# Optimization experiments

Measured on AMD Instinct MI355X. Metric: run time of the kernel, lower is better.

The kernel has to match this reference:

```python
import jax, jax.numpy as jnp
import numpy as np

P_DROP = 0.2  # matches nn.Dropout(0.2) in the module __init__ (forward's dropout_p arg is unused)
DROPOUT_KEY = jax.random.key(42)  # deterministic dropout mask for reproducible baseline


def setup_inputs() -> dict:
    key = jax.random.key(0)
    kq, kk, kv = jax.random.split(key, 3)
    B, Sq, Sk, D, Dv = 4, 4096, 4096, 64, 64
    return {
        "q": jax.random.normal(kq, (B, Sq, D), dtype=jnp.float32),
        "k": jax.random.normal(kk, (B, Sk, D), dtype=jnp.float32),
        "v": jax.random.normal(kv, (B, Sk, Dv), dtype=jnp.float32),
        "scale_factor": 1,
        "dropout_p": 0,
    }


def reference(q, k, v, scale_factor, dropout_p):
    # qk = q @ k^T, scaled  -> [B, Sq, Sk] (full attention matrix, as in the original)
    qk = jnp.einsum("bqd,bkd->bqk", q, k) * scale_factor
    probs = jax.nn.softmax(qk, axis=-1)
    # dropout (train-mode nn.Dropout(p=0.2)): deterministic mask, inverted scaling
    keep = jax.random.bernoulli(DROPOUT_KEY, 1.0 - P_DROP, probs.shape)
    probs = jnp.where(keep, probs / (1.0 - P_DROP), 0.0)
    # output = probs @ v -> [B, Sq, Dv]
    return jnp.einsum("bqk,bkd->bqd", probs, v)
```

## Files before the change

kernel.cpp:

```cpp
#include <hip/hip_runtime.h>
#include <hip/hip_bf16.h>
#include <stdint.h>

typedef __attribute__((ext_vector_type(8))) _Float16 f16x8;
typedef __attribute__((ext_vector_type(4))) float f32x4;

static constexpr int BATCH = 4;
static constexpr int SEQ = 4096;
static constexpr int DIM = 64;
static constexpr uint32_t KEEP_THRESH = 0xCCCCCE00u;
static constexpr int NSPLIT = 4;
static constexpr int TILES_TOTAL = SEQ / 64;
static constexpr int TILES_PER_SPLIT = TILES_TOTAL / NSPLIT;

static constexpr size_t ONUM_BYTES = (size_t)BATCH * 64 * NSPLIT * 64 * 64 * 4;
static constexpr size_t ML_BYTES   = (size_t)BATCH * 64 * NSPLIT * 64 * 2 * 4;
static constexpr size_t WS_NEEDED  = ONUM_BYTES + ML_BYTES;

__device__ __forceinline__ uint32_t rotl32(uint32_t x, int r) {
  return __builtin_rotateleft32(x, (uint32_t)r);
}

__device__ __forceinline__ bool tf_keep(uint32_t j) {
  const uint32_t k1 = 42u;
  const uint32_t k2 = 0x1BD11BDAu ^ k1;
  uint32_t x1 = j + k1;
  uint32_t x0 = x1;
  x1 = rotl32(x1, 13) ^ x0;
  x0 += x1; x1 = rotl32(x1, 15) ^ x0;
  x0 += x1; x1 = rotl32(x1, 26) ^ x0;
  x0 += x1; x1 = rotl32(x1, 6)  ^ x0;
  x0 += k1;      x1 += k2 + 1u;
  x0 += x1; x1 = rotl32(x1, 17) ^ x0;
  x0 += x1; x1 = rotl32(x1, 29) ^ x0;
  x0 += x1; x1 = rotl32(x1, 16) ^ x0;
  x0 += x1; x1 = rotl32(x1, 24) ^ x0;
  x0 += k2;      x1 += 2u;
  x0 += x1; x1 = rotl32(x1, 13) ^ x0;
  x0 += x1; x1 = rotl32(x1, 15) ^ x0;
  x0 += x1; x1 = rotl32(x1, 26) ^ x0;
  x0 += x1; x1 = rotl32(x1, 6)  ^ x0;
   x1 += k1 + 3u;
  x0 += x1; x1 = rotl32(x1, 17) ^ x0;
  x0 += x1; x1 = rotl32(x1, 29) ^ x0;
  x0 += x1; x1 = rotl32(x1, 16) ^ x0;
  x0 += x1; x1 = rotl32(x1, 24) ^ x0;
  x0 += k1;      x1 += k2 + 4u;
  x0 += x1; x1 = rotl32(x1, 13) ^ x0;
  x0 += x1; x1 = rotl32(x1, 15) ^ x0;
  x0 += x1; x1 = rotl32(x1, 26) ^ x0;
  x0 += x1; x1 = rotl32(x1, 6)  ^ x0;
  x0 += k2;      x1 += 5u;
  return (x0 ^ x1) < KEEP_THRESH;
}

template<bool PARTIAL>
__global__ __launch_bounds__(256, 4) void attn_kernel(
    const float* __restrict__ Q, const float* __restrict__ K, const float* __restrict__ V,
    const uint32_t* __restrict__ scale_raw,
    float* __restrict__ Out, float* __restrict__ onum, float* __restrict__ ml)
{
  __shared__ __align__(16) _Float16 Khi[64 * 72];
  __shared__ __align__(16) _Float16 Klo[64 * 72];
  __shared__ __align__(16) _Float16 Vld[64 * 72];
  __shared__ __align__(16) _Float16 Pld[4][16 * 72];

  const int b   = blockIdx.y;
  const int q0  = blockIdx.x * 64;
  const int tid = threadIdx.x;
  const int w    = tid >> 6;
  const int lane = tid & 63;
  const int l15  = lane & 15;
  const int l4   = lane >> 4;

  float scale;
  {
    uint32_t sb = *scale_raw;
    int e = (int)((sb >> 23) & 0xFFu);
    if (sb == 0u) scale = 0.0f;
    else if (e == 0 || e == 255) scale = (float)(int)sb;
    else scale = __uint_as_float(sb);
  }

  const int qw = q0 + w * 16;

  uint32_t rcb[4];
#pragma unroll
  for (int r = 0; r < 4; ++r)
    rcb[r] = ((uint32_t)(b * SEQ + qw + l4 * 4 + r)) * (uint32_t)SEQ;

  f16x8 aqh[2], aql[2];
#pragma unroll
  for (int c = 0; c < 2; ++c) {
    const float* qp = Q + ((size_t)(b * SEQ + qw + l15)) * DIM + l4 * 8 + 32 * c;
    f16x8 h, l;
#pragma unroll
    for (int j = 0; j < 8; ++j) {
      float f = qp[j];
      _Float16 fh = (_Float16)f;
      h[j] = fh;
      l[j] = (_Float16)(f - (float)fh);
    }
    aqh[c] = h; aql[c] = l;
  }

  float m_r[4], l_r[4];
  f32x4 Oacc[4];
#pragma unroll
  for (int r = 0; r < 4; ++r) { m_r[r] = -INFINITY; l_r[r] = 0.0f; }
#pragma unroll
  for (int n = 0; n < 4; ++n) Oacc[n] = f32x4{0.f, 0.f, 0.f, 0.f};

  const int t0 = PARTIAL ? (int)blockIdx.z * TILES_PER_SPLIT : 0;
  const int nt = PARTIAL ? TILES_PER_SPLIT : TILES_TOTAL;

  for (int kt = 0; kt < nt; ++kt) {
    const int kbase = (t0 + kt) * 64;
    __syncthreads();
#pragma unroll
    for (int i = 0; i < 4; ++i) {
      int flat = tid + i * 256;
      int row = flat >> 4;
      int col = (flat & 15) * 4;
      const float* kp = K + ((size_t)(b * SEQ + kbase + row)) * DIM + col;
      const float* vp = V + ((size_t)(b * SEQ + kbase + row)) * DIM + col;
      float4 kf = *(const float4*)kp;
      float4 vf = *(const float4*)vp;
      _Float16 h0 = (_Float16)kf.x, h1 = (_Float16)kf.y,
               h2 = (_Float16)kf.z, h3 = (_Float16)kf.w;
      *(ushort4*)&Khi[row * 72 + col] = ushort4{
        __builtin_bit_cast(unsigned short, h0), __builtin_bit_cast(unsigned short, h1),
        __builtin_bit_cast(unsigned short, h2), __builtin_bit_cast(unsigned short, h3)};
      _Float16 l0 = (_Float16)(kf.x - (float)h0), l1 = (_Float16)(kf.y - (float)h1),
               l2 = (_Float16)(kf.z - (float)h2), l3 = (_Float16)(kf.w - (float)h3);
      *(ushort4*)&Klo[row * 72 + col] = ushort4{
        __builtin_bit_cast(unsigned short, l0), __builtin_bit_cast(unsigned short, l1),
        __builtin_bit_cast(unsigned short, l2), __builtin_bit_cast(unsigned short, l3)};
      Vld[(col + 0) * 72 + row] = (_Float16)vf.x;
      Vld[(col + 1) * 72 + row] = (_Float16)vf.y;
      Vld[(col + 2) * 72 + row] = (_Float16)vf.z;
      Vld[(col + 3) * 72 + row] = (_Float16)vf.w;
    }
    __syncthreads();

    f32x4 s[4];
#pragma unroll
    for (int n = 0; n < 4; ++n) {
      f32x4 acc = f32x4{0.f, 0.f, 0.f, 0.f};
#pragma unroll
      for (int c = 0; c < 2; ++c) {
        int off = (16 * n + l15) * 72 + l4 * 8 + 32 * c;
        f16x8 bh = *(const f16x8*)&Khi[off];
        f16x8 bl = *(const f16x8*)&Klo[off];
        acc = __builtin_amdgcn_mfma_f32_16x16x32_f16(aqh[c], bh, acc, 0, 0, 0);
        acc = __builtin_amdgcn_mfma_f32_16x16x32_f16(aqh[c], bl, acc, 0, 0, 0);
        acc = __builtin_amdgcn_mfma_f32_16x16x32_f16(aql[c], bh, acc, 0, 0, 0);
      }
#pragma unroll
      for (int r = 0; r < 4; ++r) acc[r] *= scale;
      s[n] = acc;
    }

    uint32_t kbits = 0;
#pragma unroll
    for (int n = 0; n < 4; ++n) {
      uint32_t cb = (uint32_t)(kbase + l15 + 16 * n);
#pragma unroll
      for (int r = 0; r < 4; ++r) {
        if (tf_keep(rcb[r] + cb)) kbits |= (1u << (n * 4 + r));
      }
    }

    float mnew[4];
#pragma unroll
    for (int r = 0; r < 4; ++r) {
      mnew[r] = fmaxf(fmaxf(s[0][r], s[1][r]), fmaxf(s[2][r], s[3][r]));
#pragma unroll
      for (int off = 1; off < 16; off <<= 1)
        mnew[r] = fmaxf(mnew[r], __shfl_xor(mnew[r], off, 64));
    }

    float corr[4];
#pragma unroll
    for (int r = 0; r < 4; ++r) {
      float mn = fmaxf(m_r[r], mnew[r]);
      corr[r] = __expf(m_r[r] - mn);
      m_r[r] = mn;
      l_r[r] *= corr[r];
    }
#pragma unroll
    for (int n = 0; n < 4; ++n)
#pragma unroll
      for (int r = 0; r < 4; ++r) Oacc[n][r] *= corr[r];

    float psum[4] = {0.f, 0.f, 0.f, 0.f};
    _Float16* pw = &Pld[w][0];
#pragma unroll
    for (int n = 0; n < 4; ++n) {
#pragma unroll
      for (int r = 0; r < 4; ++r) {
        float e = __expf(s[n][r] - m_r[r]);
        psum[r] += e;
        float p = ((kbits >> (n * 4 + r)) & 1u) ? e : 0.0f;
        pw[(l4 * 4 + r) * 72 + l15 + 16 * n] = (_Float16)p;
      }
    }
#pragma unroll
    for (int r = 0; r < 4; ++r) {
#pragma unroll
      for (int off = 1; off < 16; off <<= 1)
        psum[r] += __shfl_xor(psum[r], off, 64);
      l_r[r] += psum[r];
    }

    asm volatile("s_waitcnt lgkmcnt(0)" ::: "memory");
    __builtin_amdgcn_sched_barrier(0);

    f16x8 pa[2];
#pragma unroll
    for (int c = 0; c < 2; ++c)
      pa[c] = *(const f16x8*)&pw[l15 * 72 + l4 * 8 + 32 * c];
#pragma unroll
    for (int n = 0; n < 4; ++n) {
#pragma unroll
      for (int c = 0; c < 2; ++c) {
        f16x8 bv = *(const f16x8*)&Vld[(l15 + 16 * n) * 72 + l4 * 8 + 32 * c];
        Oacc[n] = __builtin_amdgcn_mfma_f32_16x16x32_f16(pa[c], bv, Oacc[n], 0, 0, 0);
      }
    }
  }

  if (PARTIAL) {
    const int pb = ((b * 64 + (int)blockIdx.x) * NSPLIT + (int)blockIdx.z);
    float* op = onum + (size_t)pb * 4096;
#pragma unroll
    for (int r = 0; r < 4; ++r) {
      int row64 = w * 16 + l4 * 4 + r;
#pragma unroll
      for (int n = 0; n < 4; ++n)
        op[row64 * 64 + l15 + 16 * n] = Oacc[n][r];
      if (l15 == 0) {
        ml[(size_t)pb * 128 + row64 * 2 + 0] = m_r[r];
        ml[(size_t)pb * 128 + row64 * 2 + 1] = l_r[r];
      }
    }
  } else {
#pragma unroll
    for (int r = 0; r < 4; ++r) {
      float inv = 1.0f / (l_r[r] * 0.8f);
      int qg = qw + l4 * 4 + r;
      float* op = Out + ((size_t)(b * SEQ + qg)) * DIM + l15;
#pragma unroll
      for (int n = 0; n < 4; ++n)
        op[16 * n] = Oacc[n][r] * inv;
    }
  }
}

__global__ __launch_bounds__(256) void combine_kernel(
    const float* __restrict__ onum, const float* __restrict__ ml, float* __restrict__ Out)
{
  const int w = threadIdx.x >> 6;
  const int lane = threadIdx.x & 63;
  const int rid = blockIdx.x * 4 + w;
  const int b = rid >> 12;
  const int qrow = rid & 4095;
  const int qb = qrow >> 6;
  const int r64 = qrow & 63;
  const int pb0 = (b * 64 + qb) * NSPLIT;

  float m[NSPLIT], l[NSPLIT];
  float M = -INFINITY;
#pragma unroll
  for (int s = 0; s < NSPLIT; ++s) {
    m[s] = ml[(size_t)(pb0 + s) * 128 + r64 * 2 + 0];
    l[s] = ml[(size_t)(pb0 + s) * 128 + r64 * 2 + 1];
    M = fmaxf(M, m[s]);
  }
  float L = 0.0f, acc = 0.0f;
#pragma unroll
  for (int s = 0; s < NSPLIT; ++s) {
    float sc = __expf(m[s] - M);
    L += l[s] * sc;
    acc += onum[(size_t)(pb0 + s) * 4096 + r64 * 64 + lane] * sc;
  }
  Out[(size_t)rid * 64 + lane] = acc / (L * 0.8f);
}

extern "C" void kernel_launch(void* const* d_in, const int* in_sizes, int n_in,
                              void* d_out, int out_size, void* d_ws, size_t ws_size,
                              hipStream_t stream) {
  const float* Q = (const float*)d_in[0];
  const float* K = (const float*)d_in[1];
  const float* V = (const float*)d_in[2];
  const uint32_t* scale_raw = (const uint32_t*)d_in[3];
  float* Out = (float*)d_out;

  if (ws_size >= WS_NEEDED) {
    float* onum = (float*)d_ws;
    float* ml = (float*)((char*)d_ws + ONUM_BYTES);
    attn_kernel<true><<<dim3(64, BATCH, NSPLIT), 256, 0, stream>>>(
        Q, K, V, scale_raw, nullptr, onum, ml);
    combine_kernel<<<SEQ * BATCH / 4, 256, 0, stream>>>(onum, ml, Out);
  } else {
    attn_kernel<false><<<dim3(64, BATCH, 1), 256, 0, stream>>>(
        Q, K, V, scale_raw, Out, nullptr, nullptr);
  }
}
```

Measured before the change: 197.9 us.

## Swizzle LDS layouts, use ds_swizzle reductions, skip rescale, split KV eightfold

Replaces padded LDS arrays with XOR-swizzled 64-wide layouts for K hi/lo, a transposed V and P, to avoid bank conflicts and cut LDS footprint. V is now loaded column-wise so each thread writes a contiguous ushort4 into the transposed tile instead of four scalar stores. Row max and sum reductions use ds_swizzle instead of shfl_xor, the online-softmax rescale is skipped when no row max grows, and rotations use alignbit. The KV split goes from 4 to 8 when workspace allows, with launch bounds raised to 5 waves, which means more partial traffic in the combine step in exchange for more parallelism.

Result: slower. 228.1 us (+15.3%).

```diff
diff --git a/kernel.cpp b/kernel.cpp
--- a/kernel.cpp
+++ b/kernel.cpp
@@ -9,61 +9,75 @@
 static constexpr int SEQ = 4096;
 static constexpr int DIM = 64;
 static constexpr uint32_t KEEP_THRESH = 0xCCCCCE00u;
-static constexpr int NSPLIT = 4;
-static constexpr int TILES_TOTAL = SEQ / 64;
-static constexpr int TILES_PER_SPLIT = TILES_TOTAL / NSPLIT;
-
-static constexpr size_t ONUM_BYTES = (size_t)BATCH * 64 * NSPLIT * 64 * 64 * 4;
-static constexpr size_t ML_BYTES   = (size_t)BATCH * 64 * NSPLIT * 64 * 2 * 4;
-static constexpr size_t WS_NEEDED  = ONUM_BYTES + ML_BYTES;
-
-__device__ __forceinline__ uint32_t rotl32(uint32_t x, int r) {
-  return __builtin_rotateleft32(x, (uint32_t)r);
-}
+
+static constexpr size_t PB_BYTES = (64 * 64 + 128) * 4;
+static __host__ __device__ constexpr size_t ws_need(int ns) {
+  return (size_t)BATCH * 64 * ns * PB_BYTES;
+}
+static __host__ __device__ constexpr size_t onum_bytes(int ns) {
+  return (size_t)BATCH * 64 * ns * 64 * 64 * 4;
+}
+
+__device__ __forceinline__ int lds_swz(int row, int colbyte) {
+  return row * 128 + (colbyte ^ ((row & 7) << 4));
+}
+
+#define ROTL(x, r) (__builtin_amdgcn_alignbit((x), (x), 32 - (r)))
 
 __device__ __forceinline__ bool tf_keep(uint32_t j) {
   const uint32_t k1 = 42u;
   const uint32_t k2 = 0x1BD11BDAu ^ k1;
   uint32_t x1 = j + k1;
   uint32_t x0 = x1;
-  x1 = rotl32(x1, 13) ^ x0;
-  x0 += x1; x1 = rotl32(x1, 15) ^ x0;
-  x0 += x1; x1 = rotl32(x1, 26) ^ x0;
-  x0 += x1; x1 = rotl32(x1, 6)  ^ x0;
+  x1 = ROTL(x1, 13) ^ x0;
+  x0 += x1; x1 = ROTL(x1, 15) ^ x0;
+  x0 += x1; x1 = ROTL(x1, 26) ^ x0;
+  x0 += x1; x1 = ROTL(x1, 6)  ^ x0;
   x0 += k1;      x1 += k2 + 1u;
-  x0 += x1; x1 = rotl32(x1, 17) ^ x0;
-  x0 += x1; x1 = rotl32(x1, 29) ^ x0;
-  x0 += x1; x1 = rotl32(x1, 16) ^ x0;
-  x0 += x1; x1 = rotl32(x1, 24) ^ x0;
+  x0 += x1; x1 = ROTL(x1, 17) ^ x0;
+  x0 += x1; x1 = ROTL(x1, 29) ^ x0;
+  x0 += x1; x1 = ROTL(x1, 16) ^ x0;
+  x0 += x1; x1 = ROTL(x1, 24) ^ x0;
   x0 += k2;      x1 += 2u;
-  x0 += x1; x1 = rotl32(x1, 13) ^ x0;
-  x0 += x1; x1 = rotl32(x1, 15) ^ x0;
-  x0 += x1; x1 = rotl32(x1, 26) ^ x0;
-  x0 += x1; x1 = rotl32(x1, 6)  ^ x0;
-   x1 += k1 + 3u;
-  x0 += x1; x1 = rotl32(x1, 17) ^ x0;
-  x0 += x1; x1 = rotl32(x1, 29) ^ x0;
-  x0 += x1; x1 = rotl32(x1, 16) ^ x0;
-  x0 += x1; x1 = rotl32(x1, 24) ^ x0;
+  x0 += x1; x1 = ROTL(x1, 13) ^ x0;
+  x0 += x1; x1 = ROTL(x1, 15) ^ x0;
+  x0 += x1; x1 = ROTL(x1, 26) ^ x0;
+  x0 += x1; x1 = ROTL(x1, 6)  ^ x0;
+    x1 += k1 + 3u;
+  x0 += x1; x1 = ROTL(x1, 17) ^ x0;
+  x0 += x1; x1 = ROTL(x1, 29) ^ x0;
+  x0 += x1; x1 = ROTL(x1, 16) ^ x0;
+  x0 += x1; x1 = ROTL(x1, 24) ^ x0;
   x0 += k1;      x1 += k2 + 4u;
-  x0 += x1; x1 = rotl32(x1, 13) ^ x0;
-  x0 += x1; x1 = rotl32(x1, 15) ^ x0;
-  x0 += x1; x1 = rotl32(x1, 26) ^ x0;
-  x0 += x1; x1 = rotl32(x1, 6)  ^ x0;
+  x0 += x1; x1 = ROTL(x1, 13) ^ x0;
+  x0 += x1; x1 = ROTL(x1, 15) ^ x0;
+  x0 += x1; x1 = ROTL(x1, 26) ^ x0;
+  x0 += x1; x1 = ROTL(x1, 6)  ^ x0;
   x0 += k2;      x1 += 5u;
   return (x0 ^ x1) < KEEP_THRESH;
 }
 
-template<bool PARTIAL>
-__global__ __launch_bounds__(256, 4) void attn_kernel(
+template<int IMM>
+__device__ __forceinline__ float swz_max(float x) {
+  int y = __builtin_amdgcn_ds_swizzle(__float_as_int(x), IMM);
+  return fmaxf(x, __int_as_float(y));
+}
+template<int IMM>
+__device__ __forceinline__ float swz_add(float x) {
+  int y = __builtin_amdgcn_ds_swizzle(__float_as_int(x), IMM);
+  return x + __int_as_float(y);
+}
+
+template<bool PARTIAL, int NS>
+__global__ __launch_bounds__(256, 5) void attn_kernel(
     const float* __restrict__ Q, const float* __restrict__ K, const float* __restrict__ V,
     const uint32_t* __restrict__ scale_raw,
     float* __restrict__ Out, float* __restrict__ onum, float* __restrict__ ml)
 {
-  __shared__ __align__(16) _Float16 Khi[64 * 72];
-  __shared__ __align__(16) _Float16 Klo[64 * 72];
-  __shared__ __align__(16) _Float16 Vld[64 * 72];
-  __shared__ __align__(16) _Float16 Pld[4][16 * 72];
+  __shared__ __align__(16) _Float16 Khi[64 * 64];
+  __shared__ __align__(16) _Float16 Klo[64 * 64];
+  __shared__ __align__(16) _Float16 Vt[64 * 64];
+  __shared__ __align__(16) _Float16 Pld[4][16 * 64];
 
   const int b   = blockIdx.y;
   const int q0  = blockIdx.x * 64;
@@ -111,35 +125,40 @@
 #pragma unroll
   for (int n = 0; n < 4; ++n) Oacc[n] = f32x4{0.f, 0.f, 0.f, 0.f};
 
-  const int t0 = PARTIAL ? (int)blockIdx.z * TILES_PER_SPLIT : 0;
-  const int nt = PARTIAL ? TILES_PER_SPLIT : TILES_TOTAL;
+  const int nt = PARTIAL ? (SEQ / 64) / NS : SEQ / 64;
+  const int t0 = PARTIAL ? (int)blockIdx.z * nt : 0;
+
+  const int vd = tid & 63;
+  const int vq = tid >> 6;
 
   for (int kt = 0; kt < nt; ++kt) {
     const int kbase = (t0 + kt) * 64;
     __syncthreads();
 #pragma unroll
     for (int i = 0; i < 4; ++i) {
-      int flat = tid + i * 256;
-      int row = flat >> 4;
-      int col = (flat & 15) * 4;
-      const float* kp = K + ((size_t)(b * SEQ + kbase + row)) * DIM + col;
-      const float* vp = V + ((size_t)(b * SEQ + kbase + row)) * DIM + col;
-      float4 kf = *(const float4*)kp;
-      float4 vf = *(const float4*)vp;
+      int k  = (tid >> 4) + 16 * i;
+      int d0 = (tid & 15) * 4;
+      float4 kf = *(const float4*)(K + ((size_t)(b * SEQ + kbase + k)) * DIM + d0);
       _Float16 h0 = (_Float16)kf.x, h1 = (_Float16)kf.y,
                h2 = (_Float16)kf.z, h3 = (_Float16)kf.w;
-      *(ushort4*)&Khi[row * 72 + col] = ushort4{
+      *(ushort4*)((char*)Khi + lds_swz(k, d0 * 2)) = ushort4{
         __builtin_bit_cast(unsigned short, h0), __builtin_bit_cast(unsigned short, h1),
         __builtin_bit_cast(unsigned short, h2), __builtin_bit_cast(unsigned short, h3)};
       _Float16 l0 = (_Float16)(kf.x - (float)h0), l1 = (_Float16)(kf.y - (float)h1),
                l2 = (_Float16)(kf.z - (float)h2), l3 = (_Float16)(kf.w - (float)h3);
-      *(ushort4*)&Klo[row * 72 + col] = ushort4{
+      *(ushort4*)((char*)Klo + lds_swz(k, d0 * 2)) = ushort4{
         __builtin_bit_cast(unsigned short, l0), __builtin_bit_cast(unsigned short, l1),
         __builtin_bit_cast(unsigned short, l2), __builtin_bit_cast(unsigned short, l3)};
-      Vld[(col + 0) * 72 + row] = (_Float16)vf.x;
-      Vld[(col + 1) * 72 + row] = (_Float16)vf.y;
-      Vld[(col + 2) * 72 + row] = (_Float16)vf.z;
-      Vld[(col + 3) * 72 + row] = (_Float16)vf.w;
+    }
+#pragma unroll
+    for (int i = 0; i < 4; ++i) {
+      int k0 = vq * 4 + i * 16;
+      const float* vp = V + ((size_t)(b * SEQ + kbase + k0)) * DIM + vd;
+      float v0 = vp[0], v1 = vp[DIM], v2 = vp[2 * DIM], v3 = vp[3 * DIM];
+      _Float16 h0 = (_Float16)v0, h1 = (_Float16)v1, h2 = (_Float16)v2, h3 = (_Float16)v3;
+      *(ushort4*)((char*)Vt + lds_swz(vd, k0 * 2)) = ushort4{
+        __builtin_bit_cast(unsigned short, h0), __builtin_bit_cast(unsigned short, h1),
+        __builtin_bit_cast(unsigned short, h2), __builtin_bit_cast(unsigned short, h3)};
     }
     __syncthreads();
 
@@ -149,9 +168,9 @@
       f32x4 acc = f32x4{0.f, 0.f, 0.f, 0.f};
 #pragma unroll
       for (int c = 0; c < 2; ++c) {
-        int off = (16 * n + l15) * 72 + l4 * 8 + 32 * c;
-        f16x8 bh = *(const f16x8*)&Khi[off];
-        f16x8 bl = *(const f16x8*)&Klo[off];
+        int off = lds_swz(16 * n + l15, (l4 * 8 + 32 * c) * 2);
+        f16x8 bh = *(const f16x8*)((char*)Khi + off);
+        f16x8 bl = *(const f16x8*)((char*)Klo + off);
         acc = __builtin_amdgcn_mfma_f32_16x16x32_f16(aqh[c], bh, acc, 0, 0, 0);
         acc = __builtin_amdgcn_mfma_f32_16x16x32_f16(aqh[c], bl, acc, 0, 0, 0);
         acc = __builtin_amdgcn_mfma_f32_16x16x32_f16(aql[c], bh, acc, 0, 0, 0);
@@ -174,27 +193,30 @@
     float mnew[4];
 #pragma unroll
     for (int r = 0; r < 4; ++r) {
-      mnew[r] = fmaxf(fmaxf(s[0][r], s[1][r]), fmaxf(s[2][r], s[3][r]));
-#pragma unroll
-      for (int off = 1; off < 16; off <<= 1)
-        mnew[r] = fmaxf(mnew[r], __shfl_xor(mnew[r], off, 64));
-    }
-
-    float corr[4];
-#pragma unroll
-    for (int r = 0; r < 4; ++r) {
-      float mn = fmaxf(m_r[r], mnew[r]);
-      corr[r] = __expf(m_r[r] - mn);
-      m_r[r] = mn;
-      l_r[r] *= corr[r];
-    }
-#pragma unroll
-    for (int n = 0; n < 4; ++n)
-#pragma unroll
-      for (int r = 0; r < 4; ++r) Oacc[n][r] *= corr[r];
+      float v = fmaxf(fmaxf(s[0][r], s[1][r]), fmaxf(s[2][r], s[3][r]));
+      v = swz_max<0x041F>(v);
+      v = swz_max<0x081F>(v);
+      v = swz_max<0x101F>(v);
+      v = swz_max<0x201F>(v);
+      mnew[r] = v;
+    }
+
+    bool grow = (mnew[0] > m_r[0]) | (mnew[1] > m_r[1]) |
+                (mnew[2] > m_r[2]) | (mnew[3] > m_r[3]);
+    if (__any(grow)) {
+#pragma unroll
+      for (int r = 0; r < 4; ++r) {
+        float mn = fmaxf(m_r[r], mnew[r]);
+        float corr = __expf(m_r[r] - mn);
+        m_r[r] = mn;
+        l_r[r] *= corr;
+#pragma unroll
+        for (int n = 0; n < 4; ++n) Oacc[n][r] *= corr;
+      }
+    }
 
     float psum[4] = {0.f, 0.f, 0.f, 0.f};
-    _Float16* pw = &Pld[w][0];
+    char* pw = (char*)&Pld[w][0];
 #pragma unroll
     for (int n = 0; n < 4; ++n) {
 #pragma unroll
@@ -202,15 +224,17 @@
         float e = __expf(s[n][r] - m_r[r]);
         psum[r] += e;
         float p = ((kbits >> (n * 4 + r)) & 1u) ? e : 0.0f;
-        pw[(l4 * 4 + r) * 72 + l15 + 16 * n] = (_Float16)p;
+        *(_Float16*)(pw + lds_swz(l4 * 4 + r, (l15 + 16 * n) * 2)) = (_Float16)p;
       }
     }
 #pragma unroll
     for (int r = 0; r < 4; ++r) {
-#pragma unroll
-      for (int off = 1; off < 16; off <<= 1)
-        psum[r] += __shfl_xor(psum[r], off, 64);
-      l_r[r] += psum[r];
+      float v = psum[r];
+      v = swz_add<0x041F>(v);
+      v = swz_add<0x081F>(v);
+      v = swz_add<0x101F>(v);
+      v = swz_add<0x201F>(v);
+      l_r[r] += v;
     }
 
     asm volatile("s_waitcnt lgkmcnt(0)" ::: "memory");
@@ -219,19 +243,19 @@
     f16x8 pa[2];
 #pragma unroll
     for (int c = 0; c < 2; ++c)
-      pa[c] = *(const f16x8*)&pw[l15 * 72 + l4 * 8 + 32 * c];
+      pa[c] = *(const f16x8*)(pw + lds_swz(l15, (l4 * 8 + 32 * c) * 2));
 #pragma unroll
     for (int n = 0; n < 4; ++n) {
 #pragma unroll
       for (int c = 0; c < 2; ++c) {
-        f16x8 bv = *(const f16x8*)&Vld[(l15 + 16 * n) * 72 + l4 * 8 + 32 * c];
+        f16x8 bv = *(const f16x8*)((char*)Vt + lds_swz(l15 + 16 * n, (l4 * 8 + 32 * c) * 2));
         Oacc[n] = __builtin_amdgcn_mfma_f32_16x16x32_f16(pa[c], bv, Oacc[n], 0, 0, 0);
       }
     }
   }
 
   if (PARTIAL) {
-    const int pb = ((b * 64 + (int)blockIdx.x) * NSPLIT + (int)blockIdx.z);
+    const int pb = ((b * 64 + (int)blockIdx.x) * NS + (int)blockIdx.z);
     float* op = onum + (size_t)pb * 4096;
 #pragma unroll
     for (int r = 0; r < 4; ++r) {
@@ -257,6 +281,7 @@
   }
 }
 
+template<int NS>
 __global__ __launch_bounds__(256) void combine_kernel(
     const float* __restrict__ onum, const float* __restrict__ ml, float* __restrict__ Out)
 {
@@ -267,19 +292,19 @@
   const int qrow = rid & 4095;
   const int qb = qrow >> 6;
   const int r64 = qrow & 63;
-  const int pb0 = (b * 64 + qb) * NSPLIT;
-
-  float m[NSPLIT], l[NSPLIT];
+  const int pb0 = (b * 64 + qb) * NS;
+
+  float m[NS], l[NS];
   float M = -INFINITY;
 #pragma unroll
-  for (int s = 0; s < NSPLIT; ++s) {
+  for (int s = 0; s < NS; ++s) {
     m[s] = ml[(size_t)(pb0 + s) * 128 + r64 * 2 + 0];
     l[s] = ml[(size_t)(pb0 + s) * 128 + r64 * 2 + 1];
     M = fmaxf(M, m[s]);
   }
   float L = 0.0f, acc = 0.0f;
 #pragma unroll
-  for (int s = 0; s < NSPLIT; ++s) {
+  for (int s = 0; s < NS; ++s) {
     float sc = __expf(m[s] - M);
     L += l[s] * sc;
     acc += onum[(size_t)(pb0 + s) * 4096 + r64 * 64 + lane] * sc;
@@ -296,14 +321,20 @@
   const uint32_t* scale_raw = (const uint32_t*)d_in[3];
   float* Out = (float*)d_out;
 
-  if (ws_size >= WS_NEEDED) {
+  if (ws_size >= ws_need(8)) {
     float* onum = (float*)d_ws;
-    float* ml = (float*)((char*)d_ws + ONUM_BYTES);
-    attn_kernel<true><<<dim3(64, BATCH, NSPLIT), 256, 0, stream>>>(
+    float* ml = (float*)((char*)d_ws + onum_bytes(8));
+    attn_kernel<true, 8><<<dim3(64, BATCH, 8), 256, 0, stream>>>(
         Q, K, V, scale_raw, nullptr, onum, ml);
-    combine_kernel<<<SEQ * BATCH / 4, 256, 0, stream>>>(onum, ml, Out);
+    combine_kernel<8><<<SEQ * BATCH / 4, 256, 0, stream>>>(onum, ml, Out);
+  } else if (ws_size >= ws_need(4)) {
+    float* onum = (float*)d_ws;
+    float* ml = (float*)((char*)d_ws + onum_bytes(4));
+    attn_kernel<true, 4><<<dim3(64, BATCH, 4), 256, 0, stream>>>(
+        Q, K, V, scale_raw, nullptr, onum, ml);
+    combine_kernel<4><<<SEQ * BATCH / 4, 256, 0, stream>>>(onum, ml, Out);
   } else {
-    attn_kernel<false><<<dim3(64, BATCH, 1), 256, 0, stream>>>(
+    attn_kernel<false, 1><<<dim3(64, BATCH, 1), 256, 0, stream>>>(
         Q, K, V, scale_raw, Out, nullptr, nullptr);
   }
 }
```
